# Performance work log

Measured on AMD Instinct MI355X. Metric: run time of the kernel, lower is better.

## Reference

```python
import jax, jax.numpy as jnp
import numpy as np

N_NODES = 50000
N_EDGES = 600000
EMB = 128

def setup_inputs() -> dict:
    key = jax.random.key(0)
    ks = jax.random.split(key, 6)
    h = jax.random.normal(ks[0], (N_NODES, EMB), dtype=jnp.float32)
    edge_attr = jax.random.normal(ks[1], (N_EDGES, EMB), dtype=jnp.float32)
    src = jax.random.randint(ks[2], (N_EDGES,), 0, N_NODES, dtype=jnp.int32)
    dst = jax.random.randint(ks[3], (N_EDGES,), 0, N_NODES, dtype=jnp.int32)
    # MLP: Linear(emb, 2*emb) -> ReLU -> Linear(2*emb, emb)
    W1 = jax.random.normal(ks[4], (EMB, 2 * EMB), dtype=jnp.float32) * (1.0 / np.sqrt(EMB))
    b1 = jnp.zeros((2 * EMB,), dtype=jnp.float32)
    W2 = jax.random.normal(ks[5], (2 * EMB, EMB), dtype=jnp.float32) * (1.0 / np.sqrt(2 * EMB))
    b2 = jnp.zeros((EMB,), dtype=jnp.float32)
    eps = jnp.zeros((1,), dtype=jnp.float32)
    return {"h": h, "edge_attr": edge_attr, "src": src, "dst": dst,
            "W1": W1, "b1": b1, "W2": W2, "b2": b2, "eps": eps}

def reference(h, edge_attr, src, dst, W1, b1, W2, b2, eps):
    # message: m_e = h[src_e] + edge_attr_e   (edge_encoder is None)
    m = h[src] + edge_attr                              # [E, D]
    # reduce: sum messages per destination node
    aggr = jax.ops.segment_sum(m, dst, num_segments=N_NODES)  # [N, D]
    # out = (1 + eps) * h + MLP(aggr)
    hidden = jax.nn.relu(aggr @ W1 + b1)                # [N, 2D]
    mlp_out = hidden @ W2 + b2                          # [N, D]
    return (1.0 + eps) * h + mlp_out
```

## Files before the change

### kernel.cpp

```cpp
#include <hip/hip_runtime.h>
#include <hip/hip_bf16.h>

#define N_NODES 50000
#define N_EDGES 600000
#define D 128
#define H2 256
#define TN 16
#define MAXC 2048

__global__ __launch_bounds__(256) void hist_kernel(const int* __restrict__ dst,
                                                   int* __restrict__ counts) {
    unsigned int e = blockIdx.x * 256u + threadIdx.x;
    if (e < N_EDGES) atomicAdd(&counts[dst[e]], 1);
}

__global__ __launch_bounds__(256) void scan1_kernel(const int* __restrict__ counts,
                                                    int* __restrict__ scanned,
                                                    int* __restrict__ blocksums) {
    __shared__ int wsum[4];
    const int tid = threadIdx.x;
    const int lane = tid & 63;
    const int wv = tid >> 6;
    const int i = blockIdx.x * 256 + tid;
    const int cval = (i < N_NODES) ? counts[i] : 0;
    int x = cval;
    #pragma unroll
    for (int d = 1; d < 64; d <<= 1) {
        int t = __shfl_up(x, d, 64);
        if (lane >= d) x += t;
    }
    if (lane == 63) wsum[wv] = x;
    __syncthreads();
    if (tid == 0) {
        int s = 0;
        #pragma unroll
        for (int w = 0; w < 4; ++w) { s += wsum[w]; wsum[w] = s; }
    }
    __syncthreads();
    const int prefix = (wv > 0 ? wsum[wv - 1] : 0) + (x - cval);
    if (i < N_NODES) scanned[i] = prefix;
    if (tid == 0) blocksums[blockIdx.x] = wsum[3];
}

__global__ __launch_bounds__(256) void scan2_kernel(const int* __restrict__ blocksums,
                                                    int* __restrict__ blockbase, int nb) {
    __shared__ int wsum[4];
    const int tid = threadIdx.x;
    const int lane = tid & 63;
    const int wv = tid >> 6;
    const int cval = (tid < nb) ? blocksums[tid] : 0;
    int x = cval;
    #pragma unroll
    for (int d = 1; d < 64; d <<= 1) {
        int t = __shfl_up(x, d, 64);
        if (lane >= d) x += t;
    }
    if (lane == 63) wsum[wv] = x;
    __syncthreads();
    if (tid == 0) {
        int s = 0;
        #pragma unroll
        for (int w = 0; w < 4; ++w) { s += wsum[w]; wsum[w] = s; }
    }
    __syncthreads();
    if (tid < nb) blockbase[tid] = (wv > 0 ? wsum[wv - 1] : 0) + (x - cval);
}

__global__ __launch_bounds__(256) void scan3_kernel(const int* __restrict__ scanned,
                                                    const int* __restrict__ blockbase,
                                                    int* __restrict__ offsets,
                                                    int* __restrict__ cursor) {
    const int i = blockIdx.x * 256 + threadIdx.x;
    if (i < N_NODES) {
        const int v = scanned[i] + blockbase[blockIdx.x];
        offsets[i] = v;
        cursor[i] = v;
    }
    if (i == 0) offsets[N_NODES] = N_EDGES;
}

__global__ __launch_bounds__(256) void scatter_kernel(const int* __restrict__ src,
                                                      const int* __restrict__ dst,
                                                      int* __restrict__ cursor,
                                                      int2* __restrict__ perm2) {
    unsigned int e = blockIdx.x * 256u + threadIdx.x;
    if (e >= N_EDGES) return;
    const int d = dst[e];
    const int p = atomicAdd(&cursor[d], 1);
    perm2[p] = make_int2((int)e | ((d & (TN - 1)) << 20), src[e]);
}

__global__ __launch_bounds__(256) void fused_kernel(
    const float* __restrict__ h, const float* __restrict__ ea,
    const int* __restrict__ offsets, const int2* __restrict__ perm2,
    const float* __restrict__ W1, const float* __restrict__ b1,
    const float* __restrict__ W2, const float* __restrict__ b2,
    const float* __restrict__ eps, float* __restrict__ out)
{
    __shared__ float s_aggr[TN][D];
    __shared__ float s_hidden[TN][H2];
    int2* s_perm = (int2*)&s_hidden[0][0];

    const int tid = threadIdx.x;
    const int node0 = blockIdx.x * TN;

    for (int i = tid; i < TN * D / 4; i += 256)
        ((float4*)s_aggr)[i] = make_float4(0.f, 0.f, 0.f, 0.f);

    const int beg = offsets[node0];
    const int end = offsets[node0 + TN];
    const int grp = tid >> 5;
    const int c = (tid & 31) << 2;

    for (int cb = beg; cb < end; cb += MAXC) {
        const int cnt = min(end - cb, MAXC);
        __syncthreads();
        for (int i = tid; i < cnt; i += 256) s_perm[i] = perm2[cb + i];
        __syncthreads();
        const int per = (cnt + 7) >> 3;
        const int lo = grp * per;
        const int hi = min(lo + per, cnt);
        float4 acc = make_float4(0.f, 0.f, 0.f, 0.f);
        int tcur = -1;
        for (int j = lo; j < hi; ++j) {
            const int2 p = s_perm[j];
            const int t = p.x >> 20;
            const int e = p.x & 0xFFFFF;
            const float4 ev = *(const float4*)(ea + (size_t)e * D + c);
            const float4 hv = *(const float4*)(h + (size_t)p.y * D + c);
            if (t != tcur) {
                if (tcur >= 0) {
                    atomicAdd(&s_aggr[tcur][c + 0], acc.x);
                    atomicAdd(&s_aggr[tcur][c + 1], acc.y);
                    atomicAdd(&s_aggr[tcur][c + 2], acc.z);
                    atomicAdd(&s_aggr[tcur][c + 3], acc.w);
                }
                acc = make_float4(0.f, 0.f, 0.f, 0.f);
                tcur = t;
            }
            acc.x += ev.x + hv.x;
            acc.y += ev.y + hv.y;
            acc.z += ev.z + hv.z;
            acc.w += ev.w + hv.w;
        }
        if (tcur >= 0) {
            atomicAdd(&s_aggr[tcur][c + 0], acc.x);
            atomicAdd(&s_aggr[tcur][c + 1], acc.y);
            atomicAdd(&s_aggr[tcur][c + 2], acc.z);
            atomicAdd(&s_aggr[tcur][c + 3], acc.w);
        }
    }
    __syncthreads();

    {
        const int j0 = (tid & 63) << 2;
        const int tbase = (tid >> 6) << 2;
        float4 acc1[4];
        const float4 bv = *(const float4*)(b1 + j0);
        #pragma unroll
        for (int t = 0; t < 4; ++t) acc1[t] = bv;
        for (int k = 0; k < D; k += 4) {
            float4 w[4];
            #pragma unroll
            for (int q = 0; q < 4; ++q)
                w[q] = *(const float4*)(W1 + (size_t)(k + q) * H2 + j0);
            #pragma unroll
            for (int t = 0; t < 4; ++t) {
                const float4 a = *(const float4*)&s_aggr[tbase + t][k];
                acc1[t].x = fmaf(a.x, w[0].x, acc1[t].x);
                acc1[t].y = fmaf(a.x, w[0].y, acc1[t].y);
                acc1[t].z = fmaf(a.x, w[0].z, acc1[t].z);
                acc1[t].w = fmaf(a.x, w[0].w, acc1[t].w);
                acc1[t].x = fmaf(a.y, w[1].x, acc1[t].x);
                acc1[t].y = fmaf(a.y, w[1].y, acc1[t].y);
                acc1[t].z = fmaf(a.y, w[1].z, acc1[t].z);
                acc1[t].w = fmaf(a.y, w[1].w, acc1[t].w);
                acc1[t].x = fmaf(a.z, w[2].x, acc1[t].x);
                acc1[t].y = fmaf(a.z, w[2].y, acc1[t].y);
                acc1[t].z = fmaf(a.z, w[2].z, acc1[t].z);
                acc1[t].w = fmaf(a.z, w[2].w, acc1[t].w);
                acc1[t].x = fmaf(a.w, w[3].x, acc1[t].x);
                acc1[t].y = fmaf(a.w, w[3].y, acc1[t].y);
                acc1[t].z = fmaf(a.w, w[3].z, acc1[t].z);
                acc1[t].w = fmaf(a.w, w[3].w, acc1[t].w);
            }
        }
        __syncthreads();
        #pragma unroll
        for (int t = 0; t < 4; ++t) {
            float4 r;
            r.x = fmaxf(acc1[t].x, 0.f);
            r.y = fmaxf(acc1[t].y, 0.f);
            r.z = fmaxf(acc1[t].z, 0.f);
            r.w = fmaxf(acc1[t].w, 0.f);
            *(float4*)&s_hidden[tbase + t][j0] = r;
        }
    }
    __syncthreads();

    {
        const int i0 = (tid & 31) << 2;
        const int g = tid >> 5;
        float4 acc2[2];
        const float4 bv = *(const float4*)(b2 + i0);
        acc2[0] = bv; acc2[1] = bv;
        for (int k = 0; k < H2; k += 4) {
            float4 w[4];
            #pragma unroll
            for (int q = 0; q < 4; ++q)
                w[q] = *(const float4*)(W2 + (size_t)(k + q) * D + i0);
            #pragma unroll
            for (int u = 0; u < 2; ++u) {
                const float4 a = *(const float4*)&s_hidden[g + u * 8][k];
                acc2[u].x = fmaf(a.x, w[0].x, acc2[u].x);
                acc2[u].y = fmaf(a.x, w[0].y, acc2[u].y);
                acc2[u].z = fmaf(a.x, w[0].z, acc2[u].z);
                acc2[u].w = fmaf(a.x, w[0].w, acc2[u].w);
                acc2[u].x = fmaf(a.y, w[1].x, acc2[u].x);
                acc2[u].y = fmaf(a.y, w[1].y, acc2[u].y);
                acc2[u].z = fmaf(a.y, w[1].z, acc2[u].z);
                acc2[u].w = fmaf(a.y, w[1].w, acc2[u].w);
                acc2[u].x = fmaf(a.z, w[2].x, acc2[u].x);
                acc2[u].y = fmaf(a.z, w[2].y, acc2[u].y);
                acc2[u].z = fmaf(a.z, w[2].z, acc2[u].z);
                acc2[u].w = fmaf(a.z, w[2].w, acc2[u].w);
                acc2[u].x = fmaf(a.w, w[3].x, acc2[u].x);
                acc2[u].y = fmaf(a.w, w[3].y, acc2[u].y);
                acc2[u].z = fmaf(a.w, w[3].z, acc2[u].z);
                acc2[u].w = fmaf(a.w, w[3].w, acc2[u].w);
            }
        }
        const float ep = 1.0f + eps[0];
        #pragma unroll
        for (int u = 0; u < 2; ++u) {
            const int node = node0 + g + u * 8;
            const float4 hv = *(const float4*)(h + (size_t)node * D + i0);
            float4 o;
            o.x = fmaf(ep, hv.x, acc2[u].x);
            o.y = fmaf(ep, hv.y, acc2[u].y);
            o.z = fmaf(ep, hv.z, acc2[u].z);
            o.w = fmaf(ep, hv.w, acc2[u].w);
            *(float4*)(out + (size_t)node * D + i0) = o;
        }
    }
}

extern "C" void kernel_launch(void* const* d_in, const int* in_sizes, int n_in,
                              void* d_out, int out_size, void* d_ws, size_t ws_size,
                              hipStream_t stream) {
    const float* h   = (const float*)d_in[0];
    const float* ea  = (const float*)d_in[1];
    const int*   src = (const int*)d_in[2];
    const int*   dst = (const int*)d_in[3];
    const float* W1  = (const float*)d_in[4];
    const float* b1  = (const float*)d_in[5];
    const float* W2  = (const float*)d_in[6];
    const float* b2  = (const float*)d_in[7];
    const float* eps = (const float*)d_in[8];
    float* out = (float*)d_out;

    char* ws = (char*)d_ws;
    int*  counts    = (int*)ws;
    int*  scanned   = (int*)(ws + 256 * 1024);
    int*  offsets   = (int*)(ws + 512 * 1024);
    int*  cursor    = (int*)(ws + 768 * 1024);
    int*  blocksums = (int*)(ws + 1008 * 1024);
    int*  blockbase = (int*)(ws + 1012 * 1024);
    int2* perm2     = (int2*)(ws + 1024 * 1024);

    hipMemsetAsync(counts, 0, N_NODES * sizeof(int), stream);

    const int eblocks = (N_EDGES + 255) / 256;
    const int nblocks = (N_NODES + 255) / 256;

    hist_kernel<<<eblocks, 256, 0, stream>>>(dst, counts);
    scan1_kernel<<<nblocks, 256, 0, stream>>>(counts, scanned, blocksums);
    scan2_kernel<<<1, 256, 0, stream>>>(blocksums, blockbase, nblocks);
    scan3_kernel<<<nblocks, 256, 0, stream>>>(scanned, blockbase, offsets, cursor);
    scatter_kernel<<<eblocks, 256, 0, stream>>>(src, dst, cursor, perm2);
    fused_kernel<<<N_NODES / TN, 256, 0, stream>>>(
        h, ea, offsets, perm2, W1, b1, W2, b2, eps, out);
}
```

Measured before the change: 661.1 us.

## Bucket edges per 16-node tile with LDS-local counting sort and prefetched gather

Replaces the global per-node histogram, three-stage scan and global-atomic scatter with a bucket counting sort keyed by 16-node tile. It uses 64 blocks that count and scatter in shared memory, plus a column-prefix pass and a single-block scan. The fused kernel now reads per-bucket offsets and drops the run-length accumulation in favour of per-edge LDS atomics, with a 3-deep software prefetch of edge_attr/h rows. It also removes a redundant barrier. The aim is fewer launches, fewer global atomics and more memory-level parallelism in the gather. The cost is more shared-memory atomics and only 64 blocks in the sort stages. counts2d aliases perm2 in the workspace, which is safe only because bscatter reads prefix2d rather than counts2d.

```diff
diff --git a/kernel.cpp b/kernel.cpp
--- a/kernel.cpp
+++ b/kernel.cpp
@@ -1,93 +1,97 @@
 #include <hip/hip_runtime.h>
-#include <hip/hip_bf16.h>
 
 #define N_NODES 50000
 #define N_EDGES 600000
 #define D 128
 #define H2 256
 #define TN 16
+#define NBKT 3125
+#define NB 64
+#define EPB 9375
 #define MAXC 2048
 
-__global__ __launch_bounds__(256) void hist_kernel(const int* __restrict__ dst,
-                                                   int* __restrict__ counts) {
-    unsigned int e = blockIdx.x * 256u + threadIdx.x;
-    if (e < N_EDGES) atomicAdd(&counts[dst[e]], 1);
-}
-
-__global__ __launch_bounds__(256) void scan1_kernel(const int* __restrict__ counts,
-                                                    int* __restrict__ scanned,
-                                                    int* __restrict__ blocksums) {
+__global__ __launch_bounds__(256) void count_kernel(const int* __restrict__ dst,
+                                                    int* __restrict__ counts2d) {
+    __shared__ int cnt[NBKT];
+    const int b = blockIdx.x, tid = threadIdx.x;
+    for (int i = tid; i < NBKT; i += 256) cnt[i] = 0;
+    __syncthreads();
+    const int e0 = b * EPB;
+    for (int i = tid; i < EPB; i += 256)
+        atomicAdd(&cnt[dst[e0 + i] >> 4], 1);
+    __syncthreads();
+    for (int i = tid; i < NBKT; i += 256)
+        counts2d[b * NBKT + i] = cnt[i];
+}
+
+__global__ __launch_bounds__(256) void colprefix_kernel(const int* __restrict__ counts2d,
+                                                        int* __restrict__ prefix2d,
+                                                        int* __restrict__ totals) {
+    const int bin = blockIdx.x * 256 + threadIdx.x;
+    if (bin >= NBKT) return;
+    int s = 0;
+    #pragma unroll 4
+    for (int b = 0; b < NB; ++b) {
+        const int r = counts2d[b * NBKT + bin];
+        prefix2d[b * NBKT + bin] = s;
+        s += r;
+    }
+    totals[bin] = s;
+}
+
+__global__ __launch_bounds__(256) void bscan_kernel(const int* __restrict__ totals,
+                                                    int* __restrict__ offsets) {
     __shared__ int wsum[4];
+    __shared__ int carry_s;
     const int tid = threadIdx.x;
     const int lane = tid & 63;
     const int wv = tid >> 6;
-    const int i = blockIdx.x * 256 + tid;
-    const int cval = (i < N_NODES) ? counts[i] : 0;
-    int x = cval;
-    #pragma unroll
-    for (int d = 1; d < 64; d <<= 1) {
-        int t = __shfl_up(x, d, 64);
-        if (lane >= d) x += t;
-    }
-    if (lane == 63) wsum[wv] = x;
-    __syncthreads();
-    if (tid == 0) {
-        int s = 0;
-        #pragma unroll
-        for (int w = 0; w < 4; ++w) { s += wsum[w]; wsum[w] = s; }
-    }
-    __syncthreads();
-    const int prefix = (wv > 0 ? wsum[wv - 1] : 0) + (x - cval);
-    if (i < N_NODES) scanned[i] = prefix;
-    if (tid == 0) blocksums[blockIdx.x] = wsum[3];
-}
-
-__global__ __launch_bounds__(256) void scan2_kernel(const int* __restrict__ blocksums,
-                                                    int* __restrict__ blockbase, int nb) {
-    __shared__ int wsum[4];
-    const int tid = threadIdx.x;
-    const int lane = tid & 63;
-    const int wv = tid >> 6;
-    const int cval = (tid < nb) ? blocksums[tid] : 0;
-    int x = cval;
-    #pragma unroll
-    for (int d = 1; d < 64; d <<= 1) {
-        int t = __shfl_up(x, d, 64);
-        if (lane >= d) x += t;
-    }
-    if (lane == 63) wsum[wv] = x;
-    __syncthreads();
-    if (tid == 0) {
-        int s = 0;
-        #pragma unroll
-        for (int w = 0; w < 4; ++w) { s += wsum[w]; wsum[w] = s; }
-    }
-    __syncthreads();
-    if (tid < nb) blockbase[tid] = (wv > 0 ? wsum[wv - 1] : 0) + (x - cval);
-}
-
-__global__ __launch_bounds__(256) void scan3_kernel(const int* __restrict__ scanned,
-                                                    const int* __restrict__ blockbase,
-                                                    int* __restrict__ offsets,
-                                                    int* __restrict__ cursor) {
-    const int i = blockIdx.x * 256 + threadIdx.x;
-    if (i < N_NODES) {
-        const int v = scanned[i] + blockbase[blockIdx.x];
-        offsets[i] = v;
-        cursor[i] = v;
-    }
-    if (i == 0) offsets[N_NODES] = N_EDGES;
-}
-
-__global__ __launch_bounds__(256) void scatter_kernel(const int* __restrict__ src,
-                                                      const int* __restrict__ dst,
-                                                      int* __restrict__ cursor,
-                                                      int2* __restrict__ perm2) {
-    unsigned int e = blockIdx.x * 256u + threadIdx.x;
-    if (e >= N_EDGES) return;
-    const int d = dst[e];
-    const int p = atomicAdd(&cursor[d], 1);
-    perm2[p] = make_int2((int)e | ((d & (TN - 1)) << 20), src[e]);
+    if (tid == 0) carry_s = 0;
+    __syncthreads();
+    for (int base = 0; base < NBKT; base += 256) {
+        const int i = base + tid;
+        const int cval = (i < NBKT) ? totals[i] : 0;
+        int x = cval;
+        #pragma unroll
+        for (int d = 1; d < 64; d <<= 1) {
+            int t = __shfl_up(x, d, 64);
+            if (lane >= d) x += t;
+        }
+        if (lane == 63) wsum[wv] = x;
+        __syncthreads();
+        if (tid == 0) {
+            int s = 0;
+            #pragma unroll
+            for (int w = 0; w < 4; ++w) { s += wsum[w]; wsum[w] = s; }
+        }
+        __syncthreads();
+        const int carry = carry_s;
+        const int prefix = carry + (wv > 0 ? wsum[wv - 1] : 0) + (x - cval);
+        if (i < NBKT) offsets[i] = prefix;
+        __syncthreads();
+        if (tid == 0) carry_s = carry + wsum[3];
+        __syncthreads();
+    }
+    if (tid == 0) offsets[NBKT] = N_EDGES;
+}
+
+__global__ __launch_bounds__(256) void bscatter_kernel(const int* __restrict__ src,
+                                                       const int* __restrict__ dst,
+                                                       const int* __restrict__ offsets,
+                                                       const int* __restrict__ prefix2d,
+                                                       int2* __restrict__ perm2) {
+    __shared__ int lcur[NBKT];
+    const int b = blockIdx.x, tid = threadIdx.x;
+    for (int i = tid; i < NBKT; i += 256)
+        lcur[i] = offsets[i] + prefix2d[b * NBKT + i];
+    __syncthreads();
+    const int e0 = b * EPB;
+    for (int i = tid; i < EPB; i += 256) {
+        const int e = e0 + i;
+        const int d = dst[e];
+        const int pos = atomicAdd(&lcur[d >> 4], 1);
+        perm2[pos] = make_int2(e | ((d & (TN - 1)) << 20), src[e]);
+    }
 }
 
 __global__ __launch_bounds__(256) void fused_kernel(
@@ -102,13 +106,12 @@
     int2* s_perm = (int2*)&s_hidden[0][0];
 
     const int tid = threadIdx.x;
-    const int node0 = blockIdx.x * TN;
 
     for (int i = tid; i < TN * D / 4; i += 256)
         ((float4*)s_aggr)[i] = make_float4(0.f, 0.f, 0.f, 0.f);
 
-    const int beg = offsets[node0];
-    const int end = offsets[node0 + TN];
+    const int beg = offsets[blockIdx.x];
+    const int end = offsets[blockIdx.x + 1];
     const int grp = tid >> 5;
     const int c = (tid & 31) << 2;
 
@@ -120,34 +123,29 @@
         const int per = (cnt + 7) >> 3;
         const int lo = grp * per;
         const int hi = min(lo + per, cnt);
-        float4 acc = make_float4(0.f, 0.f, 0.f, 0.f);
-        int tcur = -1;
-        for (int j = lo; j < hi; ++j) {
-            const int2 p = s_perm[j];
-            const int t = p.x >> 20;
-            const int e = p.x & 0xFFFFF;
-            const float4 ev = *(const float4*)(ea + (size_t)e * D + c);
-            const float4 hv = *(const float4*)(h + (size_t)p.y * D + c);
-            if (t != tcur) {
-                if (tcur >= 0) {
-                    atomicAdd(&s_aggr[tcur][c + 0], acc.x);
-                    atomicAdd(&s_aggr[tcur][c + 1], acc.y);
-                    atomicAdd(&s_aggr[tcur][c + 2], acc.z);
-                    atomicAdd(&s_aggr[tcur][c + 3], acc.w);
-                }
-                acc = make_float4(0.f, 0.f, 0.f, 0.f);
-                tcur = t;
+        if (lo < hi) {
+            const int last = hi - 1;
+            int2 p0 = s_perm[lo];
+            int2 p1 = s_perm[min(lo + 1, last)];
+            int2 p2 = s_perm[min(lo + 2, last)];
+            float4 e0v = *(const float4*)(ea + (size_t)(p0.x & 0xFFFFF) * D + c);
+            float4 h0v = *(const float4*)(h + (size_t)p0.y * D + c);
+            float4 e1v = *(const float4*)(ea + (size_t)(p1.x & 0xFFFFF) * D + c);
+            float4 h1v = *(const float4*)(h + (size_t)p1.y * D + c);
+            #pragma unroll 2
+            for (int j = lo; j < hi; ++j) {
+                const int2 p3 = s_perm[min(j + 3, last)];
+                const float4 e2v = *(const float4*)(ea + (size_t)(p2.x & 0xFFFFF) * D + c);
+                const float4 h2v = *(const float4*)(h + (size_t)p2.y * D + c);
+                const int t = p0.x >> 20;
+                atomicAdd(&s_aggr[t][c + 0], e0v.x + h0v.x);
+                atomicAdd(&s_aggr[t][c + 1], e0v.y + h0v.y);
+                atomicAdd(&s_aggr[t][c + 2], e0v.z + h0v.z);
+                atomicAdd(&s_aggr[t][c + 3], e0v.w + h0v.w);
+                p0 = p1; e0v = e1v; h0v = h1v;
+                p1 = p2; e1v = e2v; h1v = h2v;
+                p2 = p3;
             }
-            acc.x += ev.x + hv.x;
-            acc.y += ev.y + hv.y;
-            acc.z += ev.z + hv.z;
-            acc.w += ev.w + hv.w;
-        }
-        if (tcur >= 0) {
-            atomicAdd(&s_aggr[tcur][c + 0], acc.x);
-            atomicAdd(&s_aggr[tcur][c + 1], acc.y);
-            atomicAdd(&s_aggr[tcur][c + 2], acc.z);
-            atomicAdd(&s_aggr[tcur][c + 3], acc.w);
         }
     }
     __syncthreads();
@@ -185,7 +183,6 @@
                 acc1[t].w = fmaf(a.w, w[3].w, acc1[t].w);
             }
         }
-        __syncthreads();
         #pragma unroll
         for (int t = 0; t < 4; ++t) {
             float4 r;
@@ -233,7 +230,7 @@
         const float ep = 1.0f + eps[0];
         #pragma unroll
         for (int u = 0; u < 2; ++u) {
-            const int node = node0 + g + u * 8;
+            const int node = blockIdx.x * TN + g + u * 8;
             const float4 hv = *(const float4*)(h + (size_t)node * D + i0);
             float4 o;
             o.x = fmaf(ep, hv.x, acc2[u].x);
@@ -260,24 +257,16 @@
     float* out = (float*)d_out;
 
     char* ws = (char*)d_ws;
-    int*  counts    = (int*)ws;
-    int*  scanned   = (int*)(ws + 256 * 1024);
-    int*  offsets   = (int*)(ws + 512 * 1024);
-    int*  cursor    = (int*)(ws + 768 * 1024);
-    int*  blocksums = (int*)(ws + 1008 * 1024);
-    int*  blockbase = (int*)(ws + 1012 * 1024);
-    int2* perm2     = (int2*)(ws + 1024 * 1024);
-
-    hipMemsetAsync(counts, 0, N_NODES * sizeof(int), stream);
-
-    const int eblocks = (N_EDGES + 255) / 256;
-    const int nblocks = (N_NODES + 255) / 256;
-
-    hist_kernel<<<eblocks, 256, 0, stream>>>(dst, counts);
-    scan1_kernel<<<nblocks, 256, 0, stream>>>(counts, scanned, blocksums);
-    scan2_kernel<<<1, 256, 0, stream>>>(blocksums, blockbase, nblocks);
-    scan3_kernel<<<nblocks, 256, 0, stream>>>(scanned, blockbase, offsets, cursor);
-    scatter_kernel<<<eblocks, 256, 0, stream>>>(src, dst, cursor, perm2);
-    fused_kernel<<<N_NODES / TN, 256, 0, stream>>>(
+    int2* perm2    = (int2*)ws;
+    int*  counts2d = (int*)ws;
+    int*  prefix2d = (int*)(ws + 4800000);
+    int*  totals   = (int*)(ws + 5600000);
+    int*  offsets  = (int*)(ws + 5612544);
+
+    count_kernel    <<<NB, 256, 0, stream>>>(dst, counts2d);
+    colprefix_kernel<<<(NBKT + 255) / 256, 256, 0, stream>>>(counts2d, prefix2d, totals);
+    bscan_kernel    <<<1, 256, 0, stream>>>(totals, offsets);
+    bscatter_kernel <<<NB, 256, 0, stream>>>(src, dst, offsets, prefix2d, perm2);
+    fused_kernel    <<<NBKT, 256, 0, stream>>>(
         h, ea, offsets, perm2, W1, b1, W2, b2, eps, out);
 }
```

Measured after the change: 865.1 us. +30.9%, slower.

## Aggregate each node with a dedicated 16-thread group instead of balanced edge split

Applied to the files above, without the earlier changes.

The edge aggregation now gives each of the block's 16 destination nodes its own 16-thread group. Each thread accumulates 8 columns in registers and prefetches the next edge's indices, which removes the shared-memory float atomics, the staging of edge indices into LDS, and the extra barriers. The aggregate and hidden buffers share one LDS array, which cuts shared memory per block and may raise occupancy. The cost is load imbalance: lanes in a wave wait on the highest-degree node among the four nodes that wave handles.

```diff
diff --git a/kernel.cpp b/kernel.cpp
--- a/kernel.cpp
+++ b/kernel.cpp
@@ -1,12 +1,10 @@
 #include <hip/hip_runtime.h>
-#include <hip/hip_bf16.h>
 
 #define N_NODES 50000
 #define N_EDGES 600000
 #define D 128
 #define H2 256
 #define TN 16
-#define MAXC 2048
 
 __global__ __launch_bounds__(256) void hist_kernel(const int* __restrict__ dst,
                                                    int* __restrict__ counts) {
@@ -87,7 +85,7 @@
     if (e >= N_EDGES) return;
     const int d = dst[e];
     const int p = atomicAdd(&cursor[d], 1);
-    perm2[p] = make_int2((int)e | ((d & (TN - 1)) << 20), src[e]);
+    perm2[p] = make_int2((int)e, src[e]);
 }
 
 __global__ __launch_bounds__(256) void fused_kernel(
@@ -97,58 +95,41 @@
     const float* __restrict__ W2, const float* __restrict__ b2,
     const float* __restrict__ eps, float* __restrict__ out)
 {
-    __shared__ float s_aggr[TN][D];
-    __shared__ float s_hidden[TN][H2];
-    int2* s_perm = (int2*)&s_hidden[0][0];
+    __shared__ float s_lds[TN * H2];
 
     const int tid = threadIdx.x;
-    const int node0 = blockIdx.x * TN;
-
-    for (int i = tid; i < TN * D / 4; i += 256)
-        ((float4*)s_aggr)[i] = make_float4(0.f, 0.f, 0.f, 0.f);
-
-    const int beg = offsets[node0];
-    const int end = offsets[node0 + TN];
-    const int grp = tid >> 5;
-    const int c = (tid & 31) << 2;
-
-    for (int cb = beg; cb < end; cb += MAXC) {
-        const int cnt = min(end - cb, MAXC);
-        __syncthreads();
-        for (int i = tid; i < cnt; i += 256) s_perm[i] = perm2[cb + i];
-        __syncthreads();
-        const int per = (cnt + 7) >> 3;
-        const int lo = grp * per;
-        const int hi = min(lo + per, cnt);
-        float4 acc = make_float4(0.f, 0.f, 0.f, 0.f);
-        int tcur = -1;
-        for (int j = lo; j < hi; ++j) {
-            const int2 p = s_perm[j];
-            const int t = p.x >> 20;
-            const int e = p.x & 0xFFFFF;
-            const float4 ev = *(const float4*)(ea + (size_t)e * D + c);
-            const float4 hv = *(const float4*)(h + (size_t)p.y * D + c);
-            if (t != tcur) {
-                if (tcur >= 0) {
-                    atomicAdd(&s_aggr[tcur][c + 0], acc.x);
-                    atomicAdd(&s_aggr[tcur][c + 1], acc.y);
-                    atomicAdd(&s_aggr[tcur][c + 2], acc.z);
-                    atomicAdd(&s_aggr[tcur][c + 3], acc.w);
-                }
-                acc = make_float4(0.f, 0.f, 0.f, 0.f);
-                tcur = t;
+
+    {
+        const int t  = tid >> 4;
+        const int c8 = (tid & 15) << 3;
+        const int node = blockIdx.x * TN + t;
+        const int beg = offsets[node];
+        const int end = offsets[node + 1];
+        float4 a0 = make_float4(0.f, 0.f, 0.f, 0.f);
+        float4 a1 = make_float4(0.f, 0.f, 0.f, 0.f);
+        if (beg < end) {
+            int2 p = perm2[beg];
+            for (int j = beg; j < end; ++j) {
+                const int2 pn = (j + 1 < end) ? perm2[j + 1] : p;
+                const float* er = ea + (size_t)p.x * D + c8;
+                const float* hr = h  + (size_t)p.y * D + c8;
+                const float4 e0 = *(const float4*)(er);
+                const float4 e1 = *(const float4*)(er + 4);
+                const float4 h0 = *(const float4*)(hr);
+                const float4 h1 = *(const float4*)(hr + 4);
+                a0.x += e0.x + h0.x;
+                a0.y += e0.y + h0.y;
+                a0.z += e0.z + h0.z;
+                a0.w += e0.w + h0.w;
+                a1.x += e1.x + h1.x;
+                a1.y += e1.y + h1.y;
+                a1.z += e1.z + h1.z;
+                a1.w += e1.w + h1.w;
+                p = pn;
             }
-            acc.x += ev.x + hv.x;
-            acc.y += ev.y + hv.y;
-            acc.z += ev.z + hv.z;
-            acc.w += ev.w + hv.w;
-        }
-        if (tcur >= 0) {
-            atomicAdd(&s_aggr[tcur][c + 0], acc.x);
-            atomicAdd(&s_aggr[tcur][c + 1], acc.y);
-            atomicAdd(&s_aggr[tcur][c + 2], acc.z);
-            atomicAdd(&s_aggr[tcur][c + 3], acc.w);
-        }
+        }
+        *(float4*)&s_lds[t * D + c8]     = a0;
+        *(float4*)&s_lds[t * D + c8 + 4] = a1;
     }
     __syncthreads();
 
@@ -166,7 +147,7 @@
                 w[q] = *(const float4*)(W1 + (size_t)(k + q) * H2 + j0);
             #pragma unroll
             for (int t = 0; t < 4; ++t) {
-                const float4 a = *(const float4*)&s_aggr[tbase + t][k];
+                const float4 a = *(const float4*)&s_lds[(tbase + t) * D + k];
                 acc1[t].x = fmaf(a.x, w[0].x, acc1[t].x);
                 acc1[t].y = fmaf(a.x, w[0].y, acc1[t].y);
                 acc1[t].z = fmaf(a.x, w[0].z, acc1[t].z);
@@ -193,7 +174,7 @@
             r.y = fmaxf(acc1[t].y, 0.f);
             r.z = fmaxf(acc1[t].z, 0.f);
             r.w = fmaxf(acc1[t].w, 0.f);
-            *(float4*)&s_hidden[tbase + t][j0] = r;
+            *(float4*)&s_lds[(tbase + t) * H2 + j0] = r;
         }
     }
     __syncthreads();
@@ -211,7 +192,7 @@
                 w[q] = *(const float4*)(W2 + (size_t)(k + q) * D + i0);
             #pragma unroll
             for (int u = 0; u < 2; ++u) {
-                const float4 a = *(const float4*)&s_hidden[g + u * 8][k];
+                const float4 a = *(const float4*)&s_lds[(g + u * 8) * H2 + k];
                 acc2[u].x = fmaf(a.x, w[0].x, acc2[u].x);
                 acc2[u].y = fmaf(a.x, w[0].y, acc2[u].y);
                 acc2[u].z = fmaf(a.x, w[0].z, acc2[u].z);
@@ -233,7 +214,7 @@
         const float ep = 1.0f + eps[0];
         #pragma unroll
         for (int u = 0; u < 2; ++u) {
-            const int node = node0 + g + u * 8;
+            const int node = blockIdx.x * TN + g + u * 8;
             const float4 hv = *(const float4*)(h + (size_t)node * D + i0);
             float4 o;
             o.x = fmaf(ep, hv.x, acc2[u].x);
```

Result: no change. 671.0 us (+1.5%).
